# Kernel tuning notes

Measured on AMD Instinct MI355X. Metric: run time of the kernel, lower is better.

## Reference

```python
import jax, jax.numpy as jnp
import numpy as np

E = 1024      # embed_dim
WS = 64       # window_size
B = 4
S = WS * WS   # residual add only works if seq_len == window_size**2
HID = 4 * E
EPS = 1e-5
SCALE = E ** -0.5


def _layer_norm(x, g, b):
    m = jnp.mean(x, axis=-1, keepdims=True)
    v = jnp.mean(jnp.square(x - m), axis=-1, keepdims=True)
    return (x - m) * jax.lax.rsqrt(v + EPS) * g + b


def setup_inputs() -> dict:
    key = jax.random.key(0)
    ks = jax.random.split(key, 12)
    std = 0.02
    return {
        "x":  jax.random.normal(ks[0], (B, S, E), jnp.float32),
        "Wq": jax.random.normal(ks[1], (E, E), jnp.float32) * std,
        "bq": jnp.zeros((E,), jnp.float32),
        "Wk": jax.random.normal(ks[2], (E, E), jnp.float32) * std,
        "bk": jnp.zeros((E,), jnp.float32),
        "Wv": jax.random.normal(ks[3], (E, E), jnp.float32) * std,
        "bv": jnp.zeros((E,), jnp.float32),
        "g1": jnp.ones((E,), jnp.float32),
        "be1": jnp.zeros((E,), jnp.float32),
        "W1": jax.random.normal(ks[4], (E, HID), jnp.float32) * std,
        "b1": jnp.zeros((HID,), jnp.float32),
        "W2": jax.random.normal(ks[5], (HID, E), jnp.float32) * std,
        "b2": jnp.zeros((E,), jnp.float32),
        "g2": jnp.ones((E,), jnp.float32),
        "be2": jnp.zeros((E,), jnp.float32),
    }


def reference(x, Wq, bq, Wk, bk, Wv, bv, g1, be1, W1, b1, W2, b2, g2, be2):
    b, s, e = x.shape
    n = (b * s) // (WS * WS)
    q = (x @ Wq + bq).reshape(n, WS, WS, e)
    k = (x @ Wk + bk).reshape(n, WS, WS, e)
    v = (x @ Wv + bv).reshape(n, WS, WS, e)
    # per-window attention over the last WS tokens of each (n, w) group
    scores = jnp.einsum('nwqe,nwke->nwqk', q, k) * SCALE  # (n, WS, WS, WS)
    attn = jax.nn.softmax(scores, axis=-1)
    out = jnp.einsum('nwqk,nwke->nwqe', attn, v).reshape(b, s, e)
    x = _layer_norm(x + out, g1, be1)               # dropout is identity (eval)
    ffn = jax.nn.relu(x @ W1 + b1) @ W2 + b2
    x = _layer_norm(x + ffn, g2, be2)
    return x
```

## Files before the change

### kernel.cpp

```cpp
#include <hip/hip_runtime.h>
#include <hip/hip_bf16.h>
#include <stdint.h>


typedef __attribute__((ext_vector_type(4))) float f32x4;
typedef __attribute__((ext_vector_type(8))) short bf16x8;
typedef __attribute__((ext_vector_type(4))) short bf16x4;

__device__ __forceinline__ void async_cp16(const void* g, void* l) {
    __builtin_amdgcn_global_load_lds(
        (const __attribute__((address_space(1))) void*)g,
        (__attribute__((address_space(3))) void*)l,
        16, 0, 0);
}

__device__ __forceinline__ short f2bf(float f) {
    __hip_bfloat16 h = __float2bfloat16(f);
    return __builtin_bit_cast(short, h);
}
__device__ __forceinline__ float bf2f(short s) {
    return __bfloat162float(__builtin_bit_cast(__hip_bfloat16, s));
}

template <int RELU, int MODE>
__global__ __launch_bounds__(256, 2) void gemm_kernel(
    const short* __restrict__ A, int lda,
    const short* __restrict__ Bt, int ldb,
    const float* __restrict__ bias,
    void* __restrict__ Cv, int ldc,
    int M, int N, int K)
{
    __shared__ __align__(16) short lds[8192];
    short* At  = lds;
    short* Bts = lds + 4096;

    const int t = threadIdx.x;
    const int wave = t >> 6, lane = t & 63;
    const int quad = lane >> 4, l16 = lane & 15;
    const int wx = wave & 1, wy = wave >> 1;
    const long m0 = (long)blockIdx.x * 128;
    const long n0 = (long)blockIdx.y * 128;

    const int sr = t >> 2;
    const int sc = (t & 3) << 3;

    const short* ga = A  + (m0 + sr) * (long)lda + sc;
    const short* gb = Bt + (n0 + sr) * (long)ldb + sc;
    short* la0 = At  + wave * 512;
    short* la1 = At  + 2048 + wave * 512;
    short* lb0 = Bts + wave * 512;
    short* lb1 = Bts + 2048 + wave * 512;

    f32x4 acc[4][4] = {};

    for (int k0 = 0; k0 < K; k0 += 32) {
        async_cp16(ga + k0,                  la0);
        async_cp16(ga + (long)64 * lda + k0, la1);
        async_cp16(gb + k0,                  lb0);
        async_cp16(gb + (long)64 * ldb + k0, lb1);
        __syncthreads();

        bf16x8 af[4], bfr[4];
#pragma unroll
        for (int i = 0; i < 4; ++i)
            af[i] = *(const bf16x8*)(At + (wy * 64 + i * 16 + l16) * 32 + quad * 8);
#pragma unroll
        for (int i = 0; i < 4; ++i)
            bfr[i] = *(const bf16x8*)(Bts + (wx * 64 + i * 16 + l16) * 32 + quad * 8);
#pragma unroll
        for (int mi = 0; mi < 4; ++mi)
#pragma unroll
            for (int ni = 0; ni < 4; ++ni)
                acc[mi][ni] = __builtin_amdgcn_mfma_f32_16x16x32_bf16(
                    af[mi], bfr[ni], acc[mi][ni], 0, 0, 0);
        __syncthreads();
    }

#pragma unroll
    for (int mi = 0; mi < 4; ++mi) {
#pragma unroll
        for (int ni = 0; ni < 4; ++ni) {
            const int n = (int)n0 + wx * 64 + ni * 16 + l16;
            const float bv = (MODE == 2) ? 0.f : bias[n];
#pragma unroll
            for (int r = 0; r < 4; ++r) {
                const long m = m0 + wy * 64 + mi * 16 + quad * 4 + r;
                float v = acc[mi][ni][r] + bv;
                if (MODE == 0) {
                    if (RELU) v = fmaxf(v, 0.f);
                    ((short*)Cv)[m * ldc + n] = f2bf(v);
                } else if (MODE == 1) {
                    ((float*)Cv)[m * ldc + n] = v;
                } else {
                    ((float*)Cv)[m * ldc + n] += v;
                }
            }
        }
    }
}

__global__ __launch_bounds__(256) void attn_mfma_kernel(
    const short* __restrict__ QKV, short* __restrict__ O)
{
    __shared__ __align__(16) float Sf[64 * 65];
    __shared__ __align__(16) short Pb[64 * 72];
    __shared__ __align__(16) short Vt[256 * 72];

    const int t = threadIdx.x;
    const int wave = t >> 6, lane = t & 63;
    const int quad = lane >> 4, l16 = lane & 15;
    const long rowbase = (long)blockIdx.x * 64;
    const short* Qg = QKV + rowbase * 3072;
    const short* Kg = Qg + 1024;
    const short* Vg = Qg + 2048;

    {
        const int wy = wave >> 1, wx = wave & 1;
        const short* qp0 = Qg + (long)(wy * 32 + l16) * 3072 + quad * 8;
        const short* qp1 = qp0 + 16 * 3072;
        const short* kp0 = Kg + (long)(wx * 32 + l16) * 3072 + quad * 8;
        const short* kp1 = kp0 + 16 * 3072;

        f32x4 s00 = {}, s01 = {}, s10 = {}, s11 = {};
        bf16x8 a0 = *(const bf16x8*)qp0;
        bf16x8 a1 = *(const bf16x8*)qp1;
        bf16x8 b0 = *(const bf16x8*)kp0;
        bf16x8 b1 = *(const bf16x8*)kp1;

#pragma unroll 2
        for (int k0 = 0; k0 < 1024; k0 += 32) {
            const int kn = (k0 + 32 < 1024) ? k0 + 32 : 0;
            bf16x8 na0 = *(const bf16x8*)(qp0 + kn);
            bf16x8 na1 = *(const bf16x8*)(qp1 + kn);
            bf16x8 nb0 = *(const bf16x8*)(kp0 + kn);
            bf16x8 nb1 = *(const bf16x8*)(kp1 + kn);
            s00 = __builtin_amdgcn_mfma_f32_16x16x32_bf16(a0, b0, s00, 0, 0, 0);
            s01 = __builtin_amdgcn_mfma_f32_16x16x32_bf16(a0, b1, s01, 0, 0, 0);
            s10 = __builtin_amdgcn_mfma_f32_16x16x32_bf16(a1, b0, s10, 0, 0, 0);
            s11 = __builtin_amdgcn_mfma_f32_16x16x32_bf16(a1, b1, s11, 0, 0, 0);
            a0 = na0; a1 = na1; b0 = nb0; b1 = nb1;
        }

        const int rb = wy * 32 + quad * 4;
        const int cb = wx * 32 + l16;
#pragma unroll
        for (int r = 0; r < 4; ++r) {
            Sf[(rb + r) * 65 + cb]           = s00[r] * 0.03125f;
            Sf[(rb + r) * 65 + cb + 16]      = s01[r] * 0.03125f;
            Sf[(rb + 16 + r) * 65 + cb]      = s10[r] * 0.03125f;
            Sf[(rb + 16 + r) * 65 + cb + 16] = s11[r] * 0.03125f;
        }
    }
    __syncthreads();

    {
        const int row = t >> 2;
        const int cs = (t & 3) * 16;
        const float* sp = Sf + row * 65 + cs;
        float v[16];
        float mx = -1e30f;
#pragma unroll
        for (int j = 0; j < 16; ++j) { v[j] = sp[j]; mx = fmaxf(mx, v[j]); }
        mx = fmaxf(mx, __shfl_xor(mx, 1, 64));
        mx = fmaxf(mx, __shfl_xor(mx, 2, 64));
        float sum = 0.f;
#pragma unroll
        for (int j = 0; j < 16; ++j) { v[j] = __expf(v[j] - mx); sum += v[j]; }
        sum += __shfl_xor(sum, 1, 64);
        sum += __shfl_xor(sum, 2, 64);
        const float inv = 1.f / sum;
        short* pp = Pb + row * 72 + cs;
        bf16x8 o0, o1;
#pragma unroll
        for (int j = 0; j < 8; ++j) { o0[j] = f2bf(v[j] * inv); o1[j] = f2bf(v[8 + j] * inv); }
        *(bf16x8*)(pp) = o0;
        *(bf16x8*)(pp + 8) = o1;
    }
    __syncthreads();

    bf16x8 am[2][4];
#pragma unroll
    for (int ki = 0; ki < 2; ++ki)
#pragma unroll
        for (int mi = 0; mi < 4; ++mi)
            am[ki][mi] = *(const bf16x8*)(Pb + (mi * 16 + l16) * 72 + ki * 32 + quad * 8);

    for (int nc = 0; nc < 4; ++nc) {
        const int nbase = nc * 256;
#pragma unroll
        for (int it = 0; it < 8; ++it) {
            const int idx = it * 256 + t;
            const int tok = idx >> 5;
            const int grp = idx & 31;
            bf16x8 v = *(const bf16x8*)(Vg + (long)tok * 3072 + nbase + grp * 8);
            const int tsw = tok ^ ((grp & 7) << 3);
            short* dst = Vt + (grp * 8) * 72 + tsw;
#pragma unroll
            for (int j = 0; j < 8; ++j) dst[j * 72] = v[j];
        }
        __syncthreads();

        f32x4 acc[4][4] = {};
#pragma unroll
        for (int ki = 0; ki < 2; ++ki) {
            bf16x8 bn[4];
#pragma unroll
            for (int ni = 0; ni < 4; ++ni) {
                const int e_local = wave * 64 + ni * 16 + l16;
                const int s = (e_local >> 3) & 7;
                bn[ni] = *(const bf16x8*)(Vt + e_local * 72 + ((ki * 32 + quad * 8) ^ (s << 3)));
            }
#pragma unroll
            for (int mi = 0; mi < 4; ++mi)
#pragma unroll
                for (int ni = 0; ni < 4; ++ni)
                    acc[mi][ni] = __builtin_amdgcn_mfma_f32_16x16x32_bf16(
                        am[ki][mi], bn[ni], acc[mi][ni], 0, 0, 0);
        }

#pragma unroll
        for (int mi = 0; mi < 4; ++mi)
#pragma unroll
            for (int ni = 0; ni < 4; ++ni) {
                const long n = nbase + wave * 64 + ni * 16 + l16;
#pragma unroll
                for (int r = 0; r < 4; ++r) {
                    const long m = rowbase + mi * 16 + quad * 4 + r;
                    O[m * 1024 + n] = f2bf(acc[mi][ni][r]);
                }
            }
        __syncthreads();
    }
}

__global__ __launch_bounds__(256, 4) void ln1_kernel(
    const float* __restrict__ X, const short* __restrict__ R,
    const float* __restrict__ gamma, const float* __restrict__ beta,
    short* __restrict__ Y)
{
    __shared__ float red[8];
    const int t = threadIdx.x;
    const int wave = t >> 6, lane = t & 63;
    const long row = blockIdx.x;

    f32x4 xv = *(const f32x4*)(X + row * 1024 + t * 4);
    bf16x4 rv = *(const bf16x4*)(R + row * 1024 + t * 4);
    float v[4];
    float s = 0.f, sq = 0.f;
#pragma unroll
    for (int i = 0; i < 4; ++i) {
        v[i] = xv[i] + bf2f(rv[i]);
        s += v[i];
        sq += v[i] * v[i];
    }
#pragma unroll
    for (int off = 32; off > 0; off >>= 1) {
        s  += __shfl_down(s, off, 64);
        sq += __shfl_down(sq, off, 64);
    }
    if (lane == 0) { red[wave] = s; red[4 + wave] = sq; }
    __syncthreads();
    if (t == 0) {
        float S = red[0] + red[1] + red[2] + red[3];
        float Q = red[4] + red[5] + red[6] + red[7];
        float mean = S * (1.f / 1024.f);
        float var = fmaxf(Q * (1.f / 1024.f) - mean * mean, 0.f);
        red[0] = mean;
        red[1] = rsqrtf(var + 1e-5f);
    }
    __syncthreads();
    const float mean = red[0], rstd = red[1];
    f32x4 gv = *(const f32x4*)(gamma + t * 4);
    f32x4 bv = *(const f32x4*)(beta + t * 4);
    bf16x4 yv;
#pragma unroll
    for (int i = 0; i < 4; ++i)
        yv[i] = f2bf((v[i] - mean) * rstd * gv[i] + bv[i]);
    *(bf16x4*)(Y + row * 1024 + t * 4) = yv;
}

__global__ __launch_bounds__(256, 4) void ln2_kernel(
    const short* __restrict__ X1, float* __restrict__ F,
    const float* __restrict__ gamma, const float* __restrict__ beta)
{
    __shared__ float red[8];
    const int t = threadIdx.x;
    const int wave = t >> 6, lane = t & 63;
    const long row = blockIdx.x;

    bf16x4 xv = *(const bf16x4*)(X1 + row * 1024 + t * 4);
    f32x4 fv = *(const f32x4*)(F + row * 1024 + t * 4);
    float v[4];
    float s = 0.f, sq = 0.f;
#pragma unroll
    for (int i = 0; i < 4; ++i) {
        v[i] = bf2f(xv[i]) + fv[i];
        s += v[i];
        sq += v[i] * v[i];
    }
#pragma unroll
    for (int off = 32; off > 0; off >>= 1) {
        s  += __shfl_down(s, off, 64);
        sq += __shfl_down(sq, off, 64);
    }
    if (lane == 0) { red[wave] = s; red[4 + wave] = sq; }
    __syncthreads();
    if (t == 0) {
        float S = red[0] + red[1] + red[2] + red[3];
        float Q = red[4] + red[5] + red[6] + red[7];
        float mean = S * (1.f / 1024.f);
        float var = fmaxf(Q * (1.f / 1024.f) - mean * mean, 0.f);
        red[0] = mean;
        red[1] = rsqrtf(var + 1e-5f);
    }
    __syncthreads();
    const float mean = red[0], rstd = red[1];
    f32x4 gv = *(const f32x4*)(gamma + t * 4);
    f32x4 bv = *(const f32x4*)(beta + t * 4);
    f32x4 yv;
#pragma unroll
    for (int i = 0; i < 4; ++i)
        yv[i] = (v[i] - mean) * rstd * gv[i] + bv[i];
    *(f32x4*)(F + row * 1024 + t * 4) = yv;
}

__global__ __launch_bounds__(256, 2) void transpose_kernel(
    const float* __restrict__ W, short* __restrict__ WT, int K, int N)
{
    __shared__ __align__(16) short tile[64 * 72];
    const int t = threadIdx.x;
    const long kb = (long)blockIdx.x * 64, nb = (long)blockIdx.y * 64;
    const int r = t >> 3, c = (t & 7) << 3;
#pragma unroll
    for (int i = 0; i < 2; ++i) {
        f32x4 v0 = *(const f32x4*)(W + (kb + r + i * 32) * N + nb + c);
        f32x4 v1 = *(const f32x4*)(W + (kb + r + i * 32) * N + nb + c + 4);
        short* dst = tile + (r + i * 32) * 72 + c;
#pragma unroll
        for (int j = 0; j < 4; ++j) { dst[j] = f2bf(v0[j]); dst[4 + j] = f2bf(v1[j]); }
    }
    __syncthreads();
#pragma unroll
    for (int i = 0; i < 2; ++i) {
        const int rr = r + i * 32;
        bf16x8 o;
#pragma unroll
        for (int j = 0; j < 8; ++j) o[j] = tile[(c + j) * 72 + rr];
        *(bf16x8*)(WT + (nb + rr) * K + kb + c) = o;
    }
}

__global__ __launch_bounds__(256, 4) void cvt_kernel(
    const float* __restrict__ X, short* __restrict__ Y)
{
    const long i = ((long)blockIdx.x * 256 + threadIdx.x) * 4;
    f32x4 v = *(const f32x4*)(X + i);
    bf16x4 o;
#pragma unroll
    for (int j = 0; j < 4; ++j) o[j] = f2bf(v[j]);
    *(bf16x4*)(Y + i) = o;
}

__global__ void concat_bias_kernel(const float* __restrict__ bq,
                                   const float* __restrict__ bk,
                                   const float* __restrict__ bv,
                                   float* __restrict__ out)
{
    const int i = blockIdx.x * 256 + threadIdx.x;
    float v;
    if (i < 1024)      v = bq[i];
    else if (i < 2048) v = bk[i - 1024];
    else               v = bv[i - 2048];
    out[i] = v;
}

extern "C" void kernel_launch(void* const* d_in, const int* in_sizes, int n_in,
                              void* d_out, int out_size, void* d_ws, size_t ws_size,
                              hipStream_t stream)
{
    const float* x   = (const float*)d_in[0];
    const float* Wq  = (const float*)d_in[1];
    const float* bq  = (const float*)d_in[2];
    const float* Wk  = (const float*)d_in[3];
    const float* bk  = (const float*)d_in[4];
    const float* Wv  = (const float*)d_in[5];
    const float* bv  = (const float*)d_in[6];
    const float* g1  = (const float*)d_in[7];
    const float* be1 = (const float*)d_in[8];
    const float* W1  = (const float*)d_in[9];
    const float* b1  = (const float*)d_in[10];
    const float* W2  = (const float*)d_in[11];
    const float* b2  = (const float*)d_in[12];
    const float* g2  = (const float*)d_in[13];
    const float* be2 = (const float*)d_in[14];

    const int M = in_sizes[0] / 1024;
    float* F    = (float*)d_out;
    short* xbf  = (short*)d_out;
    short* Obf  = (short*)d_out + (size_t)M * 1024;

    char* ws = (char*)d_ws;
    short* WqkvT = (short*)ws;
    short* W1T   = (short*)(ws + 6291456);
    short* W2T   = (short*)(ws + 14680064);
    float* bqkv  = (float*)(ws + 23068672);
    short* QKV   = (short*)(ws + 23080960);
    short* Hh    = (short*)(ws + 23080960);
    short* x1    = (short*)(ws + 23080960 + (size_t)M * 2048 * 2);

    dim3 blk(256);
    transpose_kernel<<<dim3(16, 16), blk, 0, stream>>>(Wq, WqkvT,               1024, 1024);
    transpose_kernel<<<dim3(16, 16), blk, 0, stream>>>(Wk, WqkvT + 1024 * 1024, 1024, 1024);
    transpose_kernel<<<dim3(16, 16), blk, 0, stream>>>(Wv, WqkvT + 2048 * 1024, 1024, 1024);
    transpose_kernel<<<dim3(16, 64), blk, 0, stream>>>(W1, W1T, 1024, 4096);
    transpose_kernel<<<dim3(64, 16), blk, 0, stream>>>(W2, W2T, 4096, 1024);
    concat_bias_kernel<<<12, blk, 0, stream>>>(bq, bk, bv, bqkv);
    cvt_kernel<<<M, blk, 0, stream>>>(x, xbf);

    gemm_kernel<0, 0><<<dim3(M / 128, 24), blk, 0, stream>>>(
        xbf, 1024, WqkvT, 1024, bqkv, QKV, 3072, M, 3072, 1024);
    attn_mfma_kernel<<<M / 64, blk, 0, stream>>>(QKV, Obf);
    ln1_kernel<<<M, blk, 0, stream>>>(x, Obf, g1, be1, x1);
    gemm_kernel<1, 0><<<dim3(M / 128, 16), blk, 0, stream>>>(
        x1, 1024, W1T, 1024, b1, Hh, 2048, M, 2048, 1024);
    gemm_kernel<0, 1><<<dim3(M / 128, 8), blk, 0, stream>>>(
        Hh, 2048, W2T, 4096, b2, F, 1024, M, 1024, 2048);
    gemm_kernel<1, 0><<<dim3(M / 128, 16), blk, 0, stream>>>(
        x1, 1024, W1T + 2048 * 1024, 1024, b1 + 2048, Hh, 2048, M, 2048, 1024);
    gemm_kernel<0, 2><<<dim3(M / 128, 8), blk, 0, stream>>>(
        Hh, 2048, W2T + 2048, 4096, b2, F, 1024, M, 1024, 2048);
    ln2_kernel<<<M, blk, 0, stream>>>(x1, F, g2, be2);
}
```

Measured before the change: 706.9 us.

## Replace 128x128 GEMM with 256x256 double-buffered, swizzled, ping-pong scheduled kernel

Replaces the simple 128x128 bf16 MFMA GEMM, which syncs twice per K=32 step, with a 512-thread 256x256 tile kernel. It double-buffers 64-wide K slices in 128KB of LDS and issues async global-to-LDS loads for the next slice between MFMA phases. It also XOR-swizzles LDS offsets to avoid bank conflicts and uses sched_barrier/setprio to interleave memory and compute. The aim is to hide global load latency and raise arithmetic intensity, at the cost of fewer blocks (M=16384 gives 64x12 or fewer tiles), a large LDS footprint and high register pressure.

```diff
diff --git a/kernel.cpp b/kernel.cpp
--- a/kernel.cpp
+++ b/kernel.cpp
@@ -23,69 +23,167 @@
 }
 
 template <int RELU, int MODE>
-__global__ __launch_bounds__(256, 2) void gemm_kernel(
+__global__ __launch_bounds__(512, 2) void gemm256_kernel(
     const short* __restrict__ A, int lda,
     const short* __restrict__ Bt, int ldb,
     const float* __restrict__ bias,
     void* __restrict__ Cv, int ldc,
     int M, int N, int K)
 {
-    __shared__ __align__(16) short lds[8192];
-    short* At  = lds;
-    short* Bts = lds + 4096;
+    __shared__ __align__(16) short lds[65536];
 
     const int t = threadIdx.x;
     const int wave = t >> 6, lane = t & 63;
     const int quad = lane >> 4, l16 = lane & 15;
-    const int wx = wave & 1, wy = wave >> 1;
-    const long m0 = (long)blockIdx.x * 128;
-    const long n0 = (long)blockIdx.y * 128;
-
-    const int sr = t >> 2;
-    const int sc = (t & 3) << 3;
-
-    const short* ga = A  + (m0 + sr) * (long)lda + sc;
-    const short* gb = Bt + (n0 + sr) * (long)ldb + sc;
-    short* la0 = At  + wave * 512;
-    short* la1 = At  + 2048 + wave * 512;
-    short* lb0 = Bts + wave * 512;
-    short* lb1 = Bts + 2048 + wave * 512;
-
-    f32x4 acc[4][4] = {};
-
-    for (int k0 = 0; k0 < K; k0 += 32) {
-        async_cp16(ga + k0,                  la0);
-        async_cp16(ga + (long)64 * lda + k0, la1);
-        async_cp16(gb + k0,                  lb0);
-        async_cp16(gb + (long)64 * ldb + k0, lb1);
-        __syncthreads();
-
-        bf16x8 af[4], bfr[4];
+    const int wm = wave >> 2, wn = wave & 3;
+    const long m0 = (long)blockIdx.x * 256;
+    const long n0 = (long)blockIdx.y * 256;
+
+    const int srow = t >> 2;
+    const int sg = t & 3;
+    const int lr0 = srow ^ ((srow >> 2) & 1);
+    const int lg0 = sg ^ (lr0 & 3);
+    const short* gA = A + (m0 + lr0) * (long)lda + lg0 * 8;
+    const short* gB = Bt + (n0 + lr0) * (long)ldb + lg0 * 8;
+    const int wdst = wave * 512;
+
+    int offA[8], offB[4];
+#pragma unroll
+    for (int mf = 0; mf < 8; ++mf) {
+        const int row = wm * 128 + mf * 16 + l16;
+        offA[mf] = (row * 32 + quad * 8) ^ ((row & 7) << 3);
+    }
+#pragma unroll
+    for (int nf = 0; nf < 4; ++nf) {
+        const int row = wn * 64 + nf * 16 + l16;
+        offB[nf] = (row * 32 + quad * 8) ^ ((row & 7) << 3);
+    }
+
+    f32x4 acc[8][4] = {};
+    const int NT = K >> 6;
+
+#define STAGE_A(ksub, kt, buf)                                                 \
+    do {                                                                       \
+        const int ko_ = (kt) * 64 + (ksub) * 32;                               \
+        short* d_ = lds + (buf) * 32768 + (ksub) * 8192 + wdst;                \
+        async_cp16(gA + ko_, d_);                                              \
+        async_cp16(gA + 128 * (long)lda + ko_, d_ + 4096);                     \
+    } while (0)
+#define STAGE_B(ksub, kt, buf)                                                 \
+    do {                                                                       \
+        const int ko_ = (kt) * 64 + (ksub) * 32;                               \
+        short* d_ = lds + (buf) * 32768 + 16384 + (ksub) * 8192 + wdst;        \
+        async_cp16(gB + ko_, d_);                                              \
+        async_cp16(gB + 128 * (long)ldb + ko_, d_ + 4096);                     \
+    } while (0)
+
+    STAGE_A(0, 0, 0); STAGE_B(0, 0, 0); STAGE_A(1, 0, 0); STAGE_B(1, 0, 0);
+    asm volatile("s_waitcnt vmcnt(4)" ::: "memory");
+    __builtin_amdgcn_s_barrier();
+    __builtin_amdgcn_sched_barrier(0);
+
+    for (int kt = 0; kt < NT; ++kt) {
+        const int cbuf = kt & 1, nbuf = cbuf ^ 1;
+        const short* Ab = lds + cbuf * 32768;
+        const short* Bb = Ab + 16384;
+        const bool more = (kt + 1 < NT);
+
+        bf16x8 av[4], bv[4];
+
+#pragma unroll
+        for (int nf = 0; nf < 4; ++nf) bv[nf] = *(const bf16x8*)(Bb + offB[nf]);
+#pragma unroll
+        for (int i = 0; i < 4; ++i) av[i] = *(const bf16x8*)(Ab + offA[i]);
+        if (more) STAGE_A(0, kt + 1, nbuf);
+        __builtin_amdgcn_sched_barrier(0);
+        __builtin_amdgcn_s_barrier();
+        asm volatile("s_waitcnt lgkmcnt(0)" ::: "memory");
+        __builtin_amdgcn_sched_barrier(0);
+        __builtin_amdgcn_s_setprio(1);
 #pragma unroll
         for (int i = 0; i < 4; ++i)
-            af[i] = *(const bf16x8*)(At + (wy * 64 + i * 16 + l16) * 32 + quad * 8);
+#pragma unroll
+            for (int nf = 0; nf < 4; ++nf)
+                acc[i][nf] = __builtin_amdgcn_mfma_f32_16x16x32_bf16(
+                    av[i], bv[nf], acc[i][nf], 0, 0, 0);
+        __builtin_amdgcn_s_setprio(0);
+        __builtin_amdgcn_sched_barrier(0);
+        __builtin_amdgcn_s_barrier();
+
+#pragma unroll
+        for (int i = 0; i < 4; ++i) av[i] = *(const bf16x8*)(Ab + offA[4 + i]);
+        if (more) STAGE_B(0, kt + 1, nbuf);
+        __builtin_amdgcn_sched_barrier(0);
+        __builtin_amdgcn_s_barrier();
+        asm volatile("s_waitcnt lgkmcnt(0)" ::: "memory");
+        __builtin_amdgcn_sched_barrier(0);
+        __builtin_amdgcn_s_setprio(1);
 #pragma unroll
         for (int i = 0; i < 4; ++i)
-            bfr[i] = *(const bf16x8*)(Bts + (wx * 64 + i * 16 + l16) * 32 + quad * 8);
-#pragma unroll
-        for (int mi = 0; mi < 4; ++mi)
-#pragma unroll
-            for (int ni = 0; ni < 4; ++ni)
-                acc[mi][ni] = __builtin_amdgcn_mfma_f32_16x16x32_bf16(
-                    af[mi], bfr[ni], acc[mi][ni], 0, 0, 0);
-        __syncthreads();
-    }
-
-#pragma unroll
-    for (int mi = 0; mi < 4; ++mi) {
-#pragma unroll
-        for (int ni = 0; ni < 4; ++ni) {
-            const int n = (int)n0 + wx * 64 + ni * 16 + l16;
-            const float bv = (MODE == 2) ? 0.f : bias[n];
+#pragma unroll
+            for (int nf = 0; nf < 4; ++nf)
+                acc[4 + i][nf] = __builtin_amdgcn_mfma_f32_16x16x32_bf16(
+                    av[i], bv[nf], acc[4 + i][nf], 0, 0, 0);
+        __builtin_amdgcn_s_setprio(0);
+        __builtin_amdgcn_sched_barrier(0);
+        if (kt == NT - 1) asm volatile("s_waitcnt vmcnt(0)" ::: "memory");
+        else              asm volatile("s_waitcnt vmcnt(4)" ::: "memory");
+        __builtin_amdgcn_s_barrier();
+        __builtin_amdgcn_sched_barrier(0);
+
+#pragma unroll
+        for (int nf = 0; nf < 4; ++nf) bv[nf] = *(const bf16x8*)(Bb + 8192 + offB[nf]);
+#pragma unroll
+        for (int i = 0; i < 4; ++i) av[i] = *(const bf16x8*)(Ab + 8192 + offA[i]);
+        if (more) STAGE_A(1, kt + 1, nbuf);
+        __builtin_amdgcn_sched_barrier(0);
+        __builtin_amdgcn_s_barrier();
+        asm volatile("s_waitcnt lgkmcnt(0)" ::: "memory");
+        __builtin_amdgcn_sched_barrier(0);
+        __builtin_amdgcn_s_setprio(1);
+#pragma unroll
+        for (int i = 0; i < 4; ++i)
+#pragma unroll
+            for (int nf = 0; nf < 4; ++nf)
+                acc[i][nf] = __builtin_amdgcn_mfma_f32_16x16x32_bf16(
+                    av[i], bv[nf], acc[i][nf], 0, 0, 0);
+        __builtin_amdgcn_s_setprio(0);
+        __builtin_amdgcn_sched_barrier(0);
+        __builtin_amdgcn_s_barrier();
+
+#pragma unroll
+        for (int i = 0; i < 4; ++i) av[i] = *(const bf16x8*)(Ab + 8192 + offA[4 + i]);
+        if (more) STAGE_B(1, kt + 1, nbuf);
+        __builtin_amdgcn_sched_barrier(0);
+        __builtin_amdgcn_s_barrier();
+        asm volatile("s_waitcnt lgkmcnt(0)" ::: "memory");
+        __builtin_amdgcn_sched_barrier(0);
+        __builtin_amdgcn_s_setprio(1);
+#pragma unroll
+        for (int i = 0; i < 4; ++i)
+#pragma unroll
+            for (int nf = 0; nf < 4; ++nf)
+                acc[4 + i][nf] = __builtin_amdgcn_mfma_f32_16x16x32_bf16(
+                    av[i], bv[nf], acc[4 + i][nf], 0, 0, 0);
+        __builtin_amdgcn_s_setprio(0);
+        __builtin_amdgcn_sched_barrier(0);
+        if (kt < NT - 1) asm volatile("s_waitcnt vmcnt(4)" ::: "memory");
+        __builtin_amdgcn_s_barrier();
+        __builtin_amdgcn_sched_barrier(0);
+    }
+#undef STAGE_A
+#undef STAGE_B
+
+#pragma unroll
+    for (int mf = 0; mf < 8; ++mf) {
+#pragma unroll
+        for (int nf = 0; nf < 4; ++nf) {
+            const int n = (int)n0 + wn * 64 + nf * 16 + l16;
+            const float bz = (MODE == 2) ? 0.f : bias[n];
 #pragma unroll
             for (int r = 0; r < 4; ++r) {
-                const long m = m0 + wy * 64 + mi * 16 + quad * 4 + r;
-                float v = acc[mi][ni][r] + bv;
+                const long m = m0 + wm * 128 + mf * 16 + quad * 4 + r;
+                float v = acc[mf][nf][r] + bz;
                 if (MODE == 0) {
                     if (RELU) v = fmaxf(v, 0.f);
                     ((short*)Cv)[m * ldc + n] = f2bf(v);
@@ -409,6 +507,7 @@
     short* x1    = (short*)(ws + 23080960 + (size_t)M * 2048 * 2);
 
     dim3 blk(256);
+    dim3 blk5(512);
     transpose_kernel<<<dim3(16, 16), blk, 0, stream>>>(Wq, WqkvT,               1024, 1024);
     transpose_kernel<<<dim3(16, 16), blk, 0, stream>>>(Wk, WqkvT + 1024 * 1024, 1024, 1024);
     transpose_kernel<<<dim3(16, 16), blk, 0, stream>>>(Wv, WqkvT + 2048 * 1024, 1024, 1024);
@@ -417,17 +516,17 @@
     concat_bias_kernel<<<12, blk, 0, stream>>>(bq, bk, bv, bqkv);
     cvt_kernel<<<M, blk, 0, stream>>>(x, xbf);
 
-    gemm_kernel<0, 0><<<dim3(M / 128, 24), blk, 0, stream>>>(
+    gemm256_kernel<0, 0><<<dim3(M / 256, 12), blk5, 0, stream>>>(
         xbf, 1024, WqkvT, 1024, bqkv, QKV, 3072, M, 3072, 1024);
     attn_mfma_kernel<<<M / 64, blk, 0, stream>>>(QKV, Obf);
     ln1_kernel<<<M, blk, 0, stream>>>(x, Obf, g1, be1, x1);
-    gemm_kernel<1, 0><<<dim3(M / 128, 16), blk, 0, stream>>>(
+    gemm256_kernel<1, 0><<<dim3(M / 256, 8), blk5, 0, stream>>>(
         x1, 1024, W1T, 1024, b1, Hh, 2048, M, 2048, 1024);
-    gemm_kernel<0, 1><<<dim3(M / 128, 8), blk, 0, stream>>>(
+    gemm256_kernel<0, 1><<<dim3(M / 256, 4), blk5, 0, stream>>>(
         Hh, 2048, W2T, 4096, b2, F, 1024, M, 1024, 2048);
-    gemm_kernel<1, 0><<<dim3(M / 128, 16), blk, 0, stream>>>(
+    gemm256_kernel<1, 0><<<dim3(M / 256, 8), blk5, 0, stream>>>(
         x1, 1024, W1T + 2048 * 1024, 1024, b1 + 2048, Hh, 2048, M, 2048, 1024);
-    gemm_kernel<0, 2><<<dim3(M / 128, 8), blk, 0, stream>>>(
+    gemm256_kernel<0, 2><<<dim3(M / 256, 4), blk5, 0, stream>>>(
         Hh, 2048, W2T + 2048, 4096, b2, F, 1024, M, 1024, 2048);
     ln2_kernel<<<M, blk, 0, stream>>>(x1, F, g2, be2);
 }
```

Result: faster. 676.3 us (-4.3%).
